# Kernel optimization log

Hardware: AMD Instinct MI355X
Metric: run time of the kernel (lower is better)

The kernel has to match this reference:

```python
import jax, jax.numpy as jnp
import numpy as np

M, N, D, P = 16, 4096, 128, 8192
H = N // D


def setup_inputs() -> dict:
    key = jax.random.key(0)
    ks = jax.random.split(key, 6)
    s = 1.0 / np.sqrt(N)
    return {
        "X": jax.random.normal(ks[0], (M, N), dtype=jnp.float32),
        "W_q": jax.random.normal(ks[1], (N, N), dtype=jnp.float32) * s,
        "W_k": jax.random.normal(ks[2], (N, N), dtype=jnp.float32) * s,
        "W_v": jax.random.normal(ks[3], (N, N), dtype=jnp.float32) * s,
        "cache_K": jax.random.normal(ks[4], (H, P, D), dtype=jnp.float32),
        "cache_V": jax.random.normal(ks[5], (H, P, D), dtype=jnp.float32),
    }


def reference(X, W_q, W_k, W_v, cache_K, cache_V):
    m = X.shape[0]
    h, p, d = cache_K.shape
    # QKV projections: [M, N] @ [N, N] -> [M, H, D] -> [H, M, D]
    q = (X @ W_q).reshape(m, h, d).transpose(1, 0, 2)
    k = (X @ W_k).reshape(m, h, d).transpose(1, 0, 2)
    v = (X @ W_v).reshape(m, h, d).transpose(1, 0, 2)
    # KV-cache concat along the sequence axis -> [H, P+M, D]
    k_all = jnp.concatenate([cache_K, k], axis=1)
    v_all = jnp.concatenate([cache_V, v], axis=1)
    # attention (note: original applies NO 1/sqrt(D) scaling)
    scores = jnp.einsum('hmd,hpd->hmp', q, k_all)  # [H, M, P+M]
    weights = jax.nn.softmax(scores, axis=-1)
    out = jnp.einsum('hmp,hpd->hmd', weights, v_all)  # [H, M, D]
    return out.transpose(1, 0, 2).reshape(m, h * d)
```

## Files before the change

### kernel.cpp

```cpp
#include <hip/hip_runtime.h>

#define HN 32
#define MM 16
#define DD 128
#define NN 4096
#define PP 8192
#define CHUNK 512
#define NCH 17
#define TP 64

#define QKV_SZ  (3*HN*MM*DD)
#define PMU_OFF QKV_SZ
#define PMU_SZ  (HN*NCH*MM)
#define PS_OFF  (PMU_OFF + PMU_SZ)
#define PACC_OFF (PS_OFF + PMU_SZ)
#define PACC_SZ (HN*NCH*MM*DD)

__global__ __launch_bounds__(256) void qkv_kernel(
    const float* __restrict__ X, const float* __restrict__ Wq,
    const float* __restrict__ Wk, const float* __restrict__ Wv,
    float* __restrict__ qkv)
{
    __shared__ float Xs[MM][128];
    const int bx  = blockIdx.x;
    const int mat = bx >> 8;
    const int r   = bx & 255;
    const int ct  = r >> 5;
    const int rc  = r & 31;
    const int col0 = ct << 9;
    const int i0   = rc << 7;
    const float* W = (mat == 0) ? Wq : (mat == 1) ? Wk : Wv;
    const int t = threadIdx.x;

    for (int f = t; f < MM*128; f += 256)
        Xs[f >> 7][f & 127] = X[(f >> 7)*NN + i0 + (f & 127)];
    __syncthreads();

    const int c0 = col0 + t, c1 = col0 + 256 + t;
    float a0[MM], a1[MM];
#pragma unroll
    for (int m = 0; m < MM; ++m) { a0[m] = 0.f; a1[m] = 0.f; }

    for (int i4 = 0; i4 < 128; i4 += 4) {
        const float* Wr = W + (size_t)(i0 + i4) * NN;
        float w00 = Wr[c0],        w01 = Wr[c1];
        float w10 = Wr[NN + c0],   w11 = Wr[NN + c1];
        float w20 = Wr[2*NN + c0], w21 = Wr[2*NN + c1];
        float w30 = Wr[3*NN + c0], w31 = Wr[3*NN + c1];
#pragma unroll
        for (int m = 0; m < MM; ++m) {
            float4 x = *reinterpret_cast<const float4*>(&Xs[m][i4]);
            a0[m] += x.x*w00 + x.y*w10 + x.z*w20 + x.w*w30;
            a1[m] += x.x*w01 + x.y*w11 + x.z*w21 + x.w*w31;
        }
    }
    float* base = qkv + (size_t)mat * HN*MM*DD;
    const int h0 = c0 >> 7, d0 = c0 & 127;
    const int h1 = c1 >> 7, d1 = c1 & 127;
#pragma unroll
    for (int m = 0; m < MM; ++m) {
        atomicAdd(&base[(h0*MM + m)*DD + d0], a0[m]);
        atomicAdd(&base[(h1*MM + m)*DD + d1], a1[m]);
    }
}

__global__ __launch_bounds__(256) void attn_partial_kernel(
    const float* __restrict__ cacheK, const float* __restrict__ cacheV,
    const float* __restrict__ qkv, float* __restrict__ pmu,
    float* __restrict__ ps, float* __restrict__ pacc)
{
    __shared__ float Qs[MM][DD];
    __shared__ float KV[TP][DD + 4];
    __shared__ __align__(16) float Ws_[TP][MM];
    __shared__ __align__(16) float mu_s[MM];
    __shared__ __align__(16) float s_s[MM];
    __shared__ __align__(16) float r_s[MM];

    const int chunk = blockIdx.x;
    const int h     = blockIdx.y;
    const int t     = threadIdx.x;

    const float* q_ws = qkv;
    const float* k_ws = qkv + HN*MM*DD;
    const float* v_ws = qkv + 2*HN*MM*DD;

    for (int f = t; f < MM*DD/4; f += 256) {
        int m = f >> 5, c4 = f & 31;
        reinterpret_cast<float4*>(&Qs[m][0])[c4] =
            reinterpret_cast<const float4*>(q_ws + (size_t)(h*MM + m)*DD)[c4];
    }
    if (t < MM) { mu_s[t] = -3.0e38f; s_s[t] = 0.0f; }

    float acc[4][8];
#pragma unroll
    for (int q = 0; q < 4; ++q)
#pragma unroll
        for (int k = 0; k < 8; ++k) acc[q][k] = 0.0f;

    const int cnt   = (chunk < 16) ? CHUNK : MM;
    const int ntile = (cnt + TP - 1) / TP;

    const int pg = t & 31, mg = t >> 5;
    const int psi = t >> 6, mgv = (t >> 4) & 3, g = t & 15;

    for (int tt = 0; tt < ntile; ++tt) {
        const int t0 = tt * TP;
        const int valid = min(TP, cnt - t0);

        __syncthreads();
        for (int f = t; f < TP*DD/4; f += 256) {
            int row = f >> 5, c4 = f & 31;
            float4 v = make_float4(0.f, 0.f, 0.f, 0.f);
            if (row < valid) {
                const float* kp = (chunk < 16)
                    ? cacheK + ((size_t)h*PP + chunk*CHUNK + t0 + row)*DD
                    : k_ws + (size_t)(h*MM + t0 + row)*DD;
                v = reinterpret_cast<const float4*>(kp)[c4];
            }
            *reinterpret_cast<float4*>(&KV[row][c4*4]) = v;
        }
        __syncthreads();
        {
            const int p0 = pg, p1 = pg + 32;
            const int m0 = mg, m1 = mg + 8;
            float s00 = 0, s01 = 0, s10 = 0, s11 = 0;
#pragma unroll 4
            for (int dq = 0; dq < DD/4; ++dq) {
                float4 k0 = *reinterpret_cast<const float4*>(&KV[p0][dq*4]);
                float4 k1 = *reinterpret_cast<const float4*>(&KV[p1][dq*4]);
                float4 q0 = *reinterpret_cast<const float4*>(&Qs[m0][dq*4]);
                float4 q1 = *reinterpret_cast<const float4*>(&Qs[m1][dq*4]);
                s00 += q0.x*k0.x + q0.y*k0.y + q0.z*k0.z + q0.w*k0.w;
                s01 += q0.x*k1.x + q0.y*k1.y + q0.z*k1.z + q0.w*k1.w;
                s10 += q1.x*k0.x + q1.y*k0.y + q1.z*k0.z + q1.w*k0.w;
                s11 += q1.x*k1.x + q1.y*k1.y + q1.z*k1.z + q1.w*k1.w;
            }
            Ws_[p0][m0] = s00;
            Ws_[p1][m0] = s01;
            Ws_[p0][m1] = s10;
            Ws_[p1][m1] = s11;
        }
        __syncthreads();
        for (int f = t; f < TP*DD/4; f += 256) {
            int row = f >> 5, c4 = f & 31;
            float4 v = make_float4(0.f, 0.f, 0.f, 0.f);
            if (row < valid) {
                const float* vp = (chunk < 16)
                    ? cacheV + ((size_t)h*PP + chunk*CHUNK + t0 + row)*DD
                    : v_ws + (size_t)(h*MM + t0 + row)*DD;
                v = reinterpret_cast<const float4*>(vp)[c4];
            }
            *reinterpret_cast<float4*>(&KV[row][c4*4]) = v;
        }
        if (t < 128) {
            const int m = t >> 3, j = t & 7;
            float mx = -3.0e38f;
            for (int p = j; p < TP; p += 8)
                if (p < valid) mx = fmaxf(mx, Ws_[p][m]);
            mx = fmaxf(mx, __shfl_xor(mx, 1));
            mx = fmaxf(mx, __shfl_xor(mx, 2));
            mx = fmaxf(mx, __shfl_xor(mx, 4));
            float mu_old = mu_s[m];
            float mu_new = fmaxf(mu_old, mx);
            float sum = 0.f;
            for (int p = j; p < TP; p += 8) {
                float w = 0.f;
                if (p < valid) w = __expf(Ws_[p][m] - mu_new);
                Ws_[p][m] = w;
                sum += w;
            }
            sum += __shfl_xor(sum, 1);
            sum += __shfl_xor(sum, 2);
            sum += __shfl_xor(sum, 4);
            if (j == 0) {
                float rr = __expf(mu_old - mu_new);
                r_s[m] = rr;
                mu_s[m] = mu_new;
                s_s[m] = s_s[m] * rr + sum;
            }
        }
        __syncthreads();
        {
            float4 rr4 = *reinterpret_cast<const float4*>(&r_s[mgv*4]);
#pragma unroll
            for (int q = 0; q < 4; ++q) {
                float rq = (&rr4.x)[q];
#pragma unroll
                for (int k = 0; k < 8; ++k) acc[q][k] *= rq;
            }
#pragma unroll 2
            for (int p = psi; p < TP; p += 4) {
                float4 w4 = *reinterpret_cast<const float4*>(&Ws_[p][mgv*4]);
                float4 v0 = *reinterpret_cast<const float4*>(&KV[p][g*8]);
                float4 v1 = *reinterpret_cast<const float4*>(&KV[p][g*8 + 4]);
#pragma unroll
                for (int q = 0; q < 4; ++q) {
                    float wq = (&w4.x)[q];
                    acc[q][0] += wq*v0.x; acc[q][1] += wq*v0.y;
                    acc[q][2] += wq*v0.z; acc[q][3] += wq*v0.w;
                    acc[q][4] += wq*v1.x; acc[q][5] += wq*v1.y;
                    acc[q][6] += wq*v1.z; acc[q][7] += wq*v1.w;
                }
            }
        }
    }

    for (int s = 0; s < 4; ++s) {
        __syncthreads();
        if (psi == s) {
#pragma unroll
            for (int q = 0; q < 4; ++q) {
                int m = mgv*4 + q;
#pragma unroll
                for (int k = 0; k < 8; ++k) {
                    if (s == 0) Qs[m][g*8 + k] = acc[q][k];
                    else        Qs[m][g*8 + k] += acc[q][k];
                }
            }
        }
    }
    __syncthreads();
    float* pa = pacc + (size_t)(h*NCH + chunk)*MM*DD;
    for (int f = t; f < MM*DD; f += 256) pa[f] = Qs[f >> 7][f & 127];
    if (t < MM) {
        pmu[(h*NCH + chunk)*MM + t] = mu_s[t];
        ps [(h*NCH + chunk)*MM + t] = s_s[t];
    }
}

__global__ __launch_bounds__(128) void combine_kernel(
    const float* __restrict__ pmu, const float* __restrict__ ps,
    const float* __restrict__ pacc, float* __restrict__ out)
{
    const int b = blockIdx.x;
    const int h = b >> 4, m = b & 15;
    const int d = threadIdx.x;
    float mu[NCH];
    float gm = -3.0e38f;
#pragma unroll
    for (int c = 0; c < NCH; ++c) {
        mu[c] = pmu[(h*NCH + c)*MM + m];
        gm = fmaxf(gm, mu[c]);
    }
    float stot = 0.f, a = 0.f;
#pragma unroll
    for (int c = 0; c < NCH; ++c) {
        float f = __expf(mu[c] - gm);
        stot += ps[(h*NCH + c)*MM + m] * f;
        a += pacc[((size_t)(h*NCH + c)*MM + m)*DD + d] * f;
    }
    out[m*NN + h*DD + d] = a / stot;
}

extern "C" void kernel_launch(void* const* d_in, const int* in_sizes, int n_in,
                              void* d_out, int out_size, void* d_ws, size_t ws_size,
                              hipStream_t stream) {
    const float* X  = (const float*)d_in[0];
    const float* Wq = (const float*)d_in[1];
    const float* Wk = (const float*)d_in[2];
    const float* Wv = (const float*)d_in[3];
    const float* cK = (const float*)d_in[4];
    const float* cV = (const float*)d_in[5];
    float* out = (float*)d_out;

    float* ws    = (float*)d_ws;
    float* qkv   = ws;
    float* pmu_p = ws + PMU_OFF;
    float* ps_p  = ws + PS_OFF;
    float* pacc_p = ws + PACC_OFF;

    hipMemsetAsync(qkv, 0, (size_t)QKV_SZ * sizeof(float), stream);
    qkv_kernel<<<768, 256, 0, stream>>>(X, Wq, Wk, Wv, qkv);
    attn_partial_kernel<<<dim3(NCH, HN), 256, 0, stream>>>(cK, cV, qkv, pmu_p, ps_p, pacc_p);
    combine_kernel<<<HN*MM, 128, 0, stream>>>(pmu_p, ps_p, pacc_p, out);
}
```

Baseline: 189.3 us.

## Split KV cache into more chunks and keep per-wave softmax state in registers

Raises the number of split-K chunks from 16 to up to 64, depending on workspace size, so the attention pass launches more blocks across the GPU. The attention kernel is restructured so each wavefront owns four query rows and one key per lane. Softmax max and sum use full-wave shuffles and the running state stays in registers, replacing shared-memory staging. The QKV projection now loads adjacent float2 columns per thread, and the final cross-wave reduction uses shuffles instead of a shared-memory pass. The cost is more partial outputs for the combine kernel to merge and Q reads straight from global memory inside the dot-product loop.

```diff
diff --git a/kernel.cpp b/kernel.cpp
--- a/kernel.cpp
+++ b/kernel.cpp
@@ -5,16 +5,7 @@
 #define DD 128
 #define NN 4096
 #define PP 8192
-#define CHUNK 512
-#define NCH 17
 #define TP 64
-
-#define QKV_SZ  (3*HN*MM*DD)
-#define PMU_OFF QKV_SZ
-#define PMU_SZ  (HN*NCH*MM)
-#define PS_OFF  (PMU_OFF + PMU_SZ)
-#define PACC_OFF (PS_OFF + PMU_SZ)
-#define PACC_SZ (HN*NCH*MM*DD)
 
 __global__ __launch_bounds__(256) void qkv_kernel(
     const float* __restrict__ X, const float* __restrict__ Wq,
@@ -36,220 +27,219 @@
         Xs[f >> 7][f & 127] = X[(f >> 7)*NN + i0 + (f & 127)];
     __syncthreads();
 
-    const int c0 = col0 + t, c1 = col0 + 256 + t;
+    const int c0 = col0 + 2*t;
     float a0[MM], a1[MM];
 #pragma unroll
     for (int m = 0; m < MM; ++m) { a0[m] = 0.f; a1[m] = 0.f; }
 
     for (int i4 = 0; i4 < 128; i4 += 4) {
-        const float* Wr = W + (size_t)(i0 + i4) * NN;
-        float w00 = Wr[c0],        w01 = Wr[c1];
-        float w10 = Wr[NN + c0],   w11 = Wr[NN + c1];
-        float w20 = Wr[2*NN + c0], w21 = Wr[2*NN + c1];
-        float w30 = Wr[3*NN + c0], w31 = Wr[3*NN + c1];
+        const float* Wr = W + (size_t)(i0 + i4) * NN + c0;
+        float2 w0 = *reinterpret_cast<const float2*>(Wr);
+        float2 w1 = *reinterpret_cast<const float2*>(Wr + NN);
+        float2 w2 = *reinterpret_cast<const float2*>(Wr + 2*NN);
+        float2 w3 = *reinterpret_cast<const float2*>(Wr + 3*NN);
 #pragma unroll
         for (int m = 0; m < MM; ++m) {
             float4 x = *reinterpret_cast<const float4*>(&Xs[m][i4]);
-            a0[m] += x.x*w00 + x.y*w10 + x.z*w20 + x.w*w30;
-            a1[m] += x.x*w01 + x.y*w11 + x.z*w21 + x.w*w31;
-        }
-    }
-    float* base = qkv + (size_t)mat * HN*MM*DD;
+            a0[m] += x.x*w0.x + x.y*w1.x + x.z*w2.x + x.w*w3.x;
+            a1[m] += x.x*w0.y + x.y*w1.y + x.z*w2.y + x.w*w3.y;
+        }
+    }
     const int h0 = c0 >> 7, d0 = c0 & 127;
-    const int h1 = c1 >> 7, d1 = c1 & 127;
+    float* base = qkv + (size_t)mat * HN*MM*DD + (size_t)h0*MM*DD + d0;
 #pragma unroll
     for (int m = 0; m < MM; ++m) {
-        atomicAdd(&base[(h0*MM + m)*DD + d0], a0[m]);
-        atomicAdd(&base[(h1*MM + m)*DD + d1], a1[m]);
-    }
-}
-
-__global__ __launch_bounds__(256) void attn_partial_kernel(
+        atomicAdd(base + m*DD,     a0[m]);
+        atomicAdd(base + m*DD + 1, a1[m]);
+    }
+}
+
+__global__ __launch_bounds__(256, 4) void attn_partial2(
     const float* __restrict__ cacheK, const float* __restrict__ cacheV,
     const float* __restrict__ qkv, float* __restrict__ pmu,
-    float* __restrict__ ps, float* __restrict__ pacc)
+    float* __restrict__ ps, float* __restrict__ pacc,
+    int nch, int chunklen)
 {
-    __shared__ float Qs[MM][DD];
     __shared__ float KV[TP][DD + 4];
-    __shared__ __align__(16) float Ws_[TP][MM];
-    __shared__ __align__(16) float mu_s[MM];
-    __shared__ __align__(16) float s_s[MM];
-    __shared__ __align__(16) float r_s[MM];
+    __shared__ float Wl[MM][68];
 
     const int chunk = blockIdx.x;
     const int h     = blockIdx.y;
     const int t     = threadIdx.x;
-
-    const float* q_ws = qkv;
+    const int lane  = t & 63;
+    const int w     = __builtin_amdgcn_readfirstlane((int)(threadIdx.x >> 6));
+    const int psi   = lane >> 4;
+    const int g     = lane & 15;
+
     const float* k_ws = qkv + HN*MM*DD;
     const float* v_ws = qkv + 2*HN*MM*DD;
-
-    for (int f = t; f < MM*DD/4; f += 256) {
-        int m = f >> 5, c4 = f & 31;
-        reinterpret_cast<float4*>(&Qs[m][0])[c4] =
-            reinterpret_cast<const float4*>(q_ws + (size_t)(h*MM + m)*DD)[c4];
-    }
-    if (t < MM) { mu_s[t] = -3.0e38f; s_s[t] = 0.0f; }
-
+    const float* qb   = qkv + (size_t)(h*MM + 4*w)*DD;
+
+    const int cnt   = (chunk < nch - 1) ? chunklen : MM;
+    const int ntile = (cnt + TP - 1) / TP;
+
+    float mu0 = -3.0e38f, mu1 = -3.0e38f, mu2 = -3.0e38f, mu3 = -3.0e38f;
+    float ss0 = 0.f, ss1 = 0.f, ss2 = 0.f, ss3 = 0.f;
     float acc[4][8];
 #pragma unroll
     for (int q = 0; q < 4; ++q)
 #pragma unroll
-        for (int k = 0; k < 8; ++k) acc[q][k] = 0.0f;
-
-    const int cnt   = (chunk < 16) ? CHUNK : MM;
-    const int ntile = (cnt + TP - 1) / TP;
-
-    const int pg = t & 31, mg = t >> 5;
-    const int psi = t >> 6, mgv = (t >> 4) & 3, g = t & 15;
+        for (int k = 0; k < 8; ++k) acc[q][k] = 0.f;
+
+    const int srow = t >> 5, sc4 = t & 31;
 
     for (int tt = 0; tt < ntile; ++tt) {
         const int t0 = tt * TP;
         const int valid = min(TP, cnt - t0);
 
         __syncthreads();
-        for (int f = t; f < TP*DD/4; f += 256) {
-            int row = f >> 5, c4 = f & 31;
+#pragma unroll
+        for (int rr = 0; rr < 8; ++rr) {
+            const int r2 = srow + rr*8;
             float4 v = make_float4(0.f, 0.f, 0.f, 0.f);
-            if (row < valid) {
-                const float* kp = (chunk < 16)
-                    ? cacheK + ((size_t)h*PP + chunk*CHUNK + t0 + row)*DD
-                    : k_ws + (size_t)(h*MM + t0 + row)*DD;
-                v = reinterpret_cast<const float4*>(kp)[c4];
+            if (r2 < valid) {
+                const float* kp = (chunk < nch - 1)
+                    ? cacheK + ((size_t)h*PP + (size_t)chunk*chunklen + t0 + r2)*DD
+                    : k_ws + (size_t)(h*MM + t0 + r2)*DD;
+                v = reinterpret_cast<const float4*>(kp)[sc4];
             }
-            *reinterpret_cast<float4*>(&KV[row][c4*4]) = v;
-        }
-        __syncthreads();
-        {
-            const int p0 = pg, p1 = pg + 32;
-            const int m0 = mg, m1 = mg + 8;
-            float s00 = 0, s01 = 0, s10 = 0, s11 = 0;
+            *reinterpret_cast<float4*>(&KV[r2][sc4*4]) = v;
+        }
+        __syncthreads();
+
+        float s0 = 0.f, s1 = 0.f, s2 = 0.f, s3 = 0.f;
+#pragma unroll 8
+        for (int dq = 0; dq < 32; ++dq) {
+            float4 k = *reinterpret_cast<const float4*>(&KV[lane][dq*4]);
+            const float* qp = qb + dq*4;
+            float4 q0 = *reinterpret_cast<const float4*>(qp);
+            float4 q1 = *reinterpret_cast<const float4*>(qp + DD);
+            float4 q2 = *reinterpret_cast<const float4*>(qp + 2*DD);
+            float4 q3 = *reinterpret_cast<const float4*>(qp + 3*DD);
+            s0 += k.x*q0.x + k.y*q0.y + k.z*q0.z + k.w*q0.w;
+            s1 += k.x*q1.x + k.y*q1.y + k.z*q1.z + k.w*q1.w;
+            s2 += k.x*q2.x + k.y*q2.y + k.z*q2.z + k.w*q2.w;
+            s3 += k.x*q3.x + k.y*q3.y + k.z*q3.z + k.w*q3.w;
+        }
+        if (lane >= valid) { s0 = s1 = s2 = s3 = -3.0e38f; }
+        __syncthreads();
+
+#pragma unroll
+        for (int rr = 0; rr < 8; ++rr) {
+            const int r2 = srow + rr*8;
+            float4 v = make_float4(0.f, 0.f, 0.f, 0.f);
+            if (r2 < valid) {
+                const float* vp = (chunk < nch - 1)
+                    ? cacheV + ((size_t)h*PP + (size_t)chunk*chunklen + t0 + r2)*DD
+                    : v_ws + (size_t)(h*MM + t0 + r2)*DD;
+                v = reinterpret_cast<const float4*>(vp)[sc4];
+            }
+            *reinterpret_cast<float4*>(&KV[r2][sc4*4]) = v;
+        }
+
+        float m0 = s0, m1 = s1, m2 = s2, m3 = s3;
+#pragma unroll
+        for (int off = 1; off < 64; off <<= 1) {
+            m0 = fmaxf(m0, __shfl_xor(m0, off));
+            m1 = fmaxf(m1, __shfl_xor(m1, off));
+            m2 = fmaxf(m2, __shfl_xor(m2, off));
+            m3 = fmaxf(m3, __shfl_xor(m3, off));
+        }
+        const float n0 = fmaxf(mu0, m0), n1 = fmaxf(mu1, m1);
+        const float n2 = fmaxf(mu2, m2), n3 = fmaxf(mu3, m3);
+        const float r0 = __expf(mu0 - n0), r1 = __expf(mu1 - n1);
+        const float r2_ = __expf(mu2 - n2), r3 = __expf(mu3 - n3);
+        float w0 = (lane < valid) ? __expf(s0 - n0) : 0.f;
+        float w1 = (lane < valid) ? __expf(s1 - n1) : 0.f;
+        float w2 = (lane < valid) ? __expf(s2 - n2) : 0.f;
+        float w3 = (lane < valid) ? __expf(s3 - n3) : 0.f;
+        float t0s = w0, t1s = w1, t2s = w2, t3s = w3;
+#pragma unroll
+        for (int off = 1; off < 64; off <<= 1) {
+            t0s += __shfl_xor(t0s, off);
+            t1s += __shfl_xor(t1s, off);
+            t2s += __shfl_xor(t2s, off);
+            t3s += __shfl_xor(t3s, off);
+        }
+        ss0 = ss0*r0 + t0s; ss1 = ss1*r1 + t1s;
+        ss2 = ss2*r2_ + t2s; ss3 = ss3*r3 + t3s;
+        mu0 = n0; mu1 = n1; mu2 = n2; mu3 = n3;
+        Wl[4*w + 0][lane] = w0;
+        Wl[4*w + 1][lane] = w1;
+        Wl[4*w + 2][lane] = w2;
+        Wl[4*w + 3][lane] = w3;
+        __syncthreads();
+
+#pragma unroll
+        for (int k = 0; k < 8; ++k) {
+            acc[0][k] *= r0; acc[1][k] *= r1; acc[2][k] *= r2_; acc[3][k] *= r3;
+        }
 #pragma unroll 4
-            for (int dq = 0; dq < DD/4; ++dq) {
-                float4 k0 = *reinterpret_cast<const float4*>(&KV[p0][dq*4]);
-                float4 k1 = *reinterpret_cast<const float4*>(&KV[p1][dq*4]);
-                float4 q0 = *reinterpret_cast<const float4*>(&Qs[m0][dq*4]);
-                float4 q1 = *reinterpret_cast<const float4*>(&Qs[m1][dq*4]);
-                s00 += q0.x*k0.x + q0.y*k0.y + q0.z*k0.z + q0.w*k0.w;
-                s01 += q0.x*k1.x + q0.y*k1.y + q0.z*k1.z + q0.w*k1.w;
-                s10 += q1.x*k0.x + q1.y*k0.y + q1.z*k0.z + q1.w*k0.w;
-                s11 += q1.x*k1.x + q1.y*k1.y + q1.z*k1.z + q1.w*k1.w;
+        for (int p = psi; p < TP; p += 4) {
+            float wq[4];
+            wq[0] = Wl[4*w + 0][p];
+            wq[1] = Wl[4*w + 1][p];
+            wq[2] = Wl[4*w + 2][p];
+            wq[3] = Wl[4*w + 3][p];
+            float4 v0 = *reinterpret_cast<const float4*>(&KV[p][g*8]);
+            float4 v1 = *reinterpret_cast<const float4*>(&KV[p][g*8 + 4]);
+#pragma unroll
+            for (int q = 0; q < 4; ++q) {
+                acc[q][0] += wq[q]*v0.x; acc[q][1] += wq[q]*v0.y;
+                acc[q][2] += wq[q]*v0.z; acc[q][3] += wq[q]*v0.w;
+                acc[q][4] += wq[q]*v1.x; acc[q][5] += wq[q]*v1.y;
+                acc[q][6] += wq[q]*v1.z; acc[q][7] += wq[q]*v1.w;
             }
-            Ws_[p0][m0] = s00;
-            Ws_[p1][m0] = s01;
-            Ws_[p0][m1] = s10;
-            Ws_[p1][m1] = s11;
-        }
-        __syncthreads();
-        for (int f = t; f < TP*DD/4; f += 256) {
-            int row = f >> 5, c4 = f & 31;
-            float4 v = make_float4(0.f, 0.f, 0.f, 0.f);
-            if (row < valid) {
-                const float* vp = (chunk < 16)
-                    ? cacheV + ((size_t)h*PP + chunk*CHUNK + t0 + row)*DD
-                    : v_ws + (size_t)(h*MM + t0 + row)*DD;
-                v = reinterpret_cast<const float4*>(vp)[c4];
-            }
-            *reinterpret_cast<float4*>(&KV[row][c4*4]) = v;
-        }
-        if (t < 128) {
-            const int m = t >> 3, j = t & 7;
-            float mx = -3.0e38f;
-            for (int p = j; p < TP; p += 8)
-                if (p < valid) mx = fmaxf(mx, Ws_[p][m]);
-            mx = fmaxf(mx, __shfl_xor(mx, 1));
-            mx = fmaxf(mx, __shfl_xor(mx, 2));
-            mx = fmaxf(mx, __shfl_xor(mx, 4));
-            float mu_old = mu_s[m];
-            float mu_new = fmaxf(mu_old, mx);
-            float sum = 0.f;
-            for (int p = j; p < TP; p += 8) {
-                float w = 0.f;
-                if (p < valid) w = __expf(Ws_[p][m] - mu_new);
-                Ws_[p][m] = w;
-                sum += w;
-            }
-            sum += __shfl_xor(sum, 1);
-            sum += __shfl_xor(sum, 2);
-            sum += __shfl_xor(sum, 4);
-            if (j == 0) {
-                float rr = __expf(mu_old - mu_new);
-                r_s[m] = rr;
-                mu_s[m] = mu_new;
-                s_s[m] = s_s[m] * rr + sum;
-            }
-        }
-        __syncthreads();
-        {
-            float4 rr4 = *reinterpret_cast<const float4*>(&r_s[mgv*4]);
-#pragma unroll
-            for (int q = 0; q < 4; ++q) {
-                float rq = (&rr4.x)[q];
-#pragma unroll
-                for (int k = 0; k < 8; ++k) acc[q][k] *= rq;
-            }
-#pragma unroll 2
-            for (int p = psi; p < TP; p += 4) {
-                float4 w4 = *reinterpret_cast<const float4*>(&Ws_[p][mgv*4]);
-                float4 v0 = *reinterpret_cast<const float4*>(&KV[p][g*8]);
-                float4 v1 = *reinterpret_cast<const float4*>(&KV[p][g*8 + 4]);
-#pragma unroll
-                for (int q = 0; q < 4; ++q) {
-                    float wq = (&w4.x)[q];
-                    acc[q][0] += wq*v0.x; acc[q][1] += wq*v0.y;
-                    acc[q][2] += wq*v0.z; acc[q][3] += wq*v0.w;
-                    acc[q][4] += wq*v1.x; acc[q][5] += wq*v1.y;
-                    acc[q][6] += wq*v1.z; acc[q][7] += wq*v1.w;
-                }
-            }
-        }
-    }
-
-    for (int s = 0; s < 4; ++s) {
-        __syncthreads();
-        if (psi == s) {
-#pragma unroll
-            for (int q = 0; q < 4; ++q) {
-                int m = mgv*4 + q;
-#pragma unroll
-                for (int k = 0; k < 8; ++k) {
-                    if (s == 0) Qs[m][g*8 + k] = acc[q][k];
-                    else        Qs[m][g*8 + k] += acc[q][k];
-                }
-            }
-        }
-    }
-    __syncthreads();
-    float* pa = pacc + (size_t)(h*NCH + chunk)*MM*DD;
-    for (int f = t; f < MM*DD; f += 256) pa[f] = Qs[f >> 7][f & 127];
-    if (t < MM) {
-        pmu[(h*NCH + chunk)*MM + t] = mu_s[t];
-        ps [(h*NCH + chunk)*MM + t] = s_s[t];
+        }
+    }
+
+#pragma unroll
+    for (int q = 0; q < 4; ++q)
+#pragma unroll
+        for (int k = 0; k < 8; ++k) {
+            float v = acc[q][k];
+            v += __shfl_xor(v, 16);
+            v += __shfl_xor(v, 32);
+            acc[q][k] = v;
+        }
+    if (psi == 0) {
+        float* pa = pacc + ((size_t)(h*nch + chunk)*MM + 4*w)*DD;
+#pragma unroll
+        for (int q = 0; q < 4; ++q) {
+            *reinterpret_cast<float4*>(pa + q*DD + g*8) =
+                make_float4(acc[q][0], acc[q][1], acc[q][2], acc[q][3]);
+            *reinterpret_cast<float4*>(pa + q*DD + g*8 + 4) =
+                make_float4(acc[q][4], acc[q][5], acc[q][6], acc[q][7]);
+        }
+    }
+    if (lane == 0) {
+        const int o = (h*nch + chunk)*MM + 4*w;
+        pmu[o + 0] = mu0; pmu[o + 1] = mu1; pmu[o + 2] = mu2; pmu[o + 3] = mu3;
+        ps [o + 0] = ss0; ps [o + 1] = ss1; ps [o + 2] = ss2; ps [o + 3] = ss3;
     }
 }
 
 __global__ __launch_bounds__(128) void combine_kernel(
     const float* __restrict__ pmu, const float* __restrict__ ps,
-    const float* __restrict__ pacc, float* __restrict__ out)
+    const float* __restrict__ pacc, float* __restrict__ out, int nch)
 {
     const int b = blockIdx.x;
     const int h = b >> 4, m = b & 15;
     const int d = threadIdx.x;
-    float mu[NCH];
     float gm = -3.0e38f;
-#pragma unroll
-    for (int c = 0; c < NCH; ++c) {
-        mu[c] = pmu[(h*NCH + c)*MM + m];
-        gm = fmaxf(gm, mu[c]);
-    }
+    for (int c = 0; c < nch; ++c)
+        gm = fmaxf(gm, pmu[(h*nch + c)*MM + m]);
     float stot = 0.f, a = 0.f;
-#pragma unroll
-    for (int c = 0; c < NCH; ++c) {
-        float f = __expf(mu[c] - gm);
-        stot += ps[(h*NCH + c)*MM + m] * f;
-        a += pacc[((size_t)(h*NCH + c)*MM + m)*DD + d] * f;
+    for (int c = 0; c < nch; ++c) {
+        const float f = __expf(pmu[(h*nch + c)*MM + m] - gm);
+        stot += ps[(h*nch + c)*MM + m] * f;
+        a += pacc[((size_t)(h*nch + c)*MM + m)*DD + d] * f;
     }
     out[m*NN + h*DD + d] = a / stot;
+}
+
+static size_t ws_need_floats(int nch) {
+    return (size_t)3*HN*MM*DD + 2*(size_t)HN*nch*MM + (size_t)HN*nch*MM*DD;
 }
 
 extern "C" void kernel_launch(void* const* d_in, const int* in_sizes, int n_in,
@@ -263,14 +253,20 @@
     const float* cV = (const float*)d_in[5];
     float* out = (float*)d_out;
 
-    float* ws    = (float*)d_ws;
-    float* qkv   = ws;
-    float* pmu_p = ws + PMU_OFF;
-    float* ps_p  = ws + PS_OFF;
-    float* pacc_p = ws + PACC_OFF;
-
-    hipMemsetAsync(qkv, 0, (size_t)QKV_SZ * sizeof(float), stream);
+    int nch = 65;
+    if (ws_size < ws_need_floats(65)*sizeof(float)) nch = 33;
+    if (ws_size < ws_need_floats(33)*sizeof(float)) nch = 17;
+    const int chunklen = PP / (nch - 1);
+
+    float* ws     = (float*)d_ws;
+    float* qkv    = ws;
+    float* pmu_p  = ws + 3*HN*MM*DD;
+    float* ps_p   = pmu_p + (size_t)HN*nch*MM;
+    float* pacc_p = ps_p + (size_t)HN*nch*MM;
+
+    hipMemsetAsync(qkv, 0, (size_t)3*HN*MM*DD*sizeof(float), stream);
     qkv_kernel<<<768, 256, 0, stream>>>(X, Wq, Wk, Wv, qkv);
-    attn_partial_kernel<<<dim3(NCH, HN), 256, 0, stream>>>(cK, cV, qkv, pmu_p, ps_p, pacc_p);
-    combine_kernel<<<HN*MM, 128, 0, stream>>>(pmu_p, ps_p, pacc_p, out);
-}
+    attn_partial2<<<dim3(nch, HN), 256, 0, stream>>>(cK, cV, qkv, pmu_p, ps_p, pacc_p,
+                                                     nch, chunklen);
+    combine_kernel<<<HN*MM, 128, 0, stream>>>(pmu_p, ps_p, pacc_p, out, nch);
+}
```

After: 205.0 us. +8.3%, slower.
